# Performance work log

Measured on AMD Instinct MI355X. Metric: run time of the kernel, lower is better.

The kernel has to match this reference:

```python
import jax, jax.numpy as jnp
import numpy as np

L, B, D, H, R, C, WIN = 256, 64, 1024, 512, 8, 6, 10
N = B * L
DH = D + H  # concat(node_features, graph output)


def _window_pairs():
    pi, pk = [], []
    for j in range(L):
        for k in range(max(0, j - WIN), min(L, j + WIN + 1)):
            pi.append(j)
            pk.append(k)
    return np.asarray(pi, np.int32), np.asarray(pk, np.int32)


def setup_inputs() -> dict:
    key = jax.random.key(0)
    ks = jax.random.split(key, 16)
    s = 0.02
    pi, pk = _window_pairs()
    return {
        "features": jax.random.normal(ks[0], (L, B, D), jnp.float32),
        "Wscalar": jax.random.normal(ks[1], (D, L), jnp.float32) * s,   # MaskedEdgeAttention scalar
        "W_rel": jax.random.normal(ks[2], (R, D, H), jnp.float32) * s,  # RGCN per-relation weights
        "W_root": jax.random.normal(ks[3], (D, H), jnp.float32) * s,
        "b_rgcn": jnp.zeros((H,), jnp.float32),
        "W_nbr": jax.random.normal(ks[4], (H, H), jnp.float32) * s,     # GraphConv neighbor weight
        "W_self": jax.random.normal(ks[5], (H, H), jnp.float32) * s,
        "b_gc": jnp.zeros((H,), jnp.float32),
        "W_match": jax.random.normal(ks[6], (DH, DH), jnp.float32) * s,  # MatchingAttention 'general2'
        "b_match": jnp.zeros((DH,), jnp.float32),
        "W_lin": jax.random.normal(ks[7], (DH, H), jnp.float32) * s,
        "b_lin": jnp.zeros((H,), jnp.float32),
        "W_fc": jax.random.normal(ks[8], (H, C), jnp.float32) * s,
        "b_fc": jnp.zeros((C,), jnp.float32),
        "speakers": jax.random.randint(ks[9], (L, B), 0, 2, jnp.int32),
        "pair_i": jnp.asarray(pi),
        "pair_k": jnp.asarray(pk),
    }


def reference(features, Wscalar, W_rel, W_root, b_rgcn, W_nbr, W_self, b_gc,
              W_match, b_match, W_lin, b_lin, W_fc, b_fc,
              speakers, pair_i, pair_k):
    # --- edge attention scores (MaskedEdgeAttention, attn1 style) ---
    scale = jnp.einsum('sbd,dm->sbm', features, Wscalar)      # [L,B,L]
    alpha = jax.nn.softmax(scale, axis=0)
    alpha = jnp.transpose(alpha, (1, 2, 0))                   # [B, anchor, src]
    win = jnp.full((L, L), 1e-10, jnp.float32).at[pair_i, pair_k].set(1.0)
    masked = alpha * win
    scores = masked / jnp.sum(masked, axis=-1, keepdims=True)  # renormalized over window
    edge_norm = scores[:, pair_i, pair_k].reshape(-1)          # [E]

    # --- batch_graphify: flatten nodes conversation-major, build global edges ---
    x = jnp.transpose(features, (1, 0, 2)).reshape(N, D)       # [N, D]
    offs = jnp.arange(B, dtype=jnp.int32)[:, None] * L
    src = (offs + pair_i[None, :]).reshape(-1)
    dst = (offs + pair_k[None, :]).reshape(-1)
    sp = speakers.T                                            # [B, L]
    dir_bit = jnp.where(pair_i < pair_k, 0, 1).astype(jnp.int32)
    rel = (sp[:, pair_i] * 4 + sp[:, pair_k] * 2 + dir_bit[None, :]).reshape(-1)

    # --- RGCNConv: per-relation transform, edge_norm-weighted sum at dst + root ---
    h_all = jnp.einsum('nd,rdh->nrh', x, W_rel)                # [N, R, H]
    msg = h_all[src, rel] * edge_norm[:, None]                 # [E, H]
    agg = jax.ops.segment_sum(msg, dst, num_segments=N)
    h1 = agg + x @ W_root + b_rgcn

    # --- GraphConv: W_nbr @ sum_j x_j + W_self @ x + b ---
    nbr = jax.ops.segment_sum(h1[src], dst, num_segments=N)
    h2 = nbr @ W_nbr + h1 @ W_self + b_gc

    # --- attentive_node_features (MatchingAttention 'general2', full-length mask=1) ---
    em = jnp.concatenate([x, h2], axis=-1).reshape(B, L, DH)
    em = jnp.transpose(em, (1, 0, 2))                          # [L, B, DH] seq-major
    xt = jnp.einsum('tbd,de->tbe', em, W_match) + b_match
    a = jax.nn.softmax(jnp.tanh(jnp.einsum('tbe,sbe->bts', xt, em)), axis=2)
    att = jnp.einsum('bts,sbd->tbd', a, em)                    # [L, B, DH]

    # --- classify_node_features (dropout = eval identity) ---
    hidden = jax.nn.relu(jnp.einsum('tbd,dh->tbh', att, W_lin) + b_lin)
    logp = jax.nn.log_softmax(hidden @ W_fc + b_fc, axis=2)    # [L, B, C]
    return jnp.transpose(logp, (1, 0, 2)).reshape(N, C)
```

## Files before the change

### kernel.cpp

```cpp
#include <hip/hip_runtime.h>
#include <hip/hip_bf16.h>

#define Lc 256
#define Bc 64
#define Dc 1024
#define Hc 512
#define Rc 8
#define Cc 6
#define WINc 10
#define NWc 21
#define Nc (Bc*Lc)
#define DHc (Dc+Hc)
#define CH 8192

typedef __attribute__((ext_vector_type(8))) short short8;
typedef __attribute__((ext_vector_type(4))) float floatx4;

__device__ inline unsigned short f2b(float x) {
    __hip_bfloat16 h = __float2bfloat16(x);
    return *reinterpret_cast<unsigned short*>(&h);
}
__device__ inline float bf2f(unsigned short u) {
    __hip_bfloat16 h;
    *reinterpret_cast<unsigned short*>(&h) = u;
    return __bfloat162float(h);
}

__device__ inline long remap_row(int node) { return (long)(((node & 255) << 6) + (node >> 8)); }

typedef __attribute__((address_space(3))) unsigned int lds_u32;
typedef __attribute__((address_space(1))) unsigned int glb_u32;
__device__ inline void glds16(const unsigned short* g, unsigned short* l) {
    __builtin_amdgcn_global_load_lds((const glb_u32*)g, (lds_u32*)l, 16, 0, 0);
}

#define SB0 __builtin_amdgcn_sched_barrier(0)
#define BAR __builtin_amdgcn_s_barrier()

__device__ __forceinline__ void xcd_remap(int gridX, int& x, int& y)
{
    int nwg = gridDim.x * gridDim.y;
    int bid = blockIdx.y * gridDim.x + blockIdx.x;
    int q = nwg >> 3, r = nwg & 7;
    int xcd = bid & 7, pos = bid >> 3;
    int logical = xcd * q + min(xcd, r) + pos;
    x = logical % gridX;
    y = logical / gridX;
}

__global__ __launch_bounds__(256) void prep_all(
    const float* __restrict__ Wscalar, const float* __restrict__ W_rel,
    const float* __restrict__ W_root, const float* __restrict__ W_nbr,
    const float* __restrict__ W_self, const float* __restrict__ W_match,
    const float* __restrict__ W_lin, unsigned short* __restrict__ WT,
    const int* __restrict__ spk, int* __restrict__ idx, int* __restrict__ cnts,
    const float* __restrict__ feats, unsigned short* __restrict__ em)
{
    int t = blockIdx.x;
    if (t >= 8448 + 16384) {
        int c = t - (8448 + 16384);
        int tid = threadIdx.x;
        int base = c * CH;
        __shared__ int zs[256];
        int zcount = 0;
        for (int i = 0; i < CH / 256; i++) {
            int n = base + tid * (CH / 256) + i;
            if (spk[(n & 255) * 64 + (n >> 8)] == 0) zcount++;
        }
        zs[tid] = zcount; __syncthreads();
        for (int off = 1; off < 256; off <<= 1) {
            int v = (tid >= off) ? zs[tid - off] : 0;
            __syncthreads();
            zs[tid] += v;
            __syncthreads();
        }
        int Z = zs[255];
        int zpos = zs[tid] - zcount;
        int opos = tid * (CH / 256) - zpos;
        for (int i = 0; i < CH / 256; i++) {
            int nl = tid * (CH / 256) + i;
            int n = base + nl;
            if (spk[(n & 255) * 64 + (n >> 8)] == 0) idx[base + (zpos++)] = nl;
            else                                     idx[base + Z + (opos++)] = nl;
        }
        if (tid == 0) cnts[c] = Z;
        return;
    }
    if (t >= 8448) {
        int n = t - 8448;
        int tid = threadIdx.x;
        const float* f = feats + remap_row(n) * Dc;
        float4 v = ((const float4*)f)[tid];
        unsigned short* e = em + (long)n * DHc + tid * 4;
        e[0] = f2b(v.x); e[1] = f2b(v.y); e[2] = f2b(v.z); e[3] = f2b(v.w);
        return;
    }
    const float* in; unsigned short* out; int N, ldo, n0, k0;
    if (t < 256) {
        in = Wscalar; out = WT; N = 256; ldo = 1024;
        n0 = (t & 7) * 32; k0 = (t >> 3) * 32;
    } else if (t < 4352) {
        int u = t - 256; int r = u >> 9; u &= 511;
        in = W_rel + (long)r * 524288; out = WT + 262144 + (long)r * 524288; N = 512; ldo = 1024;
        n0 = (u & 15) * 32; k0 = (u >> 4) * 32;
    } else if (t < 4864) {
        int u = t - 4352;
        in = W_root; out = WT + 262144 + 4096 * 1024; N = 512; ldo = 1024;
        n0 = (u & 15) * 32; k0 = (u >> 4) * 32;
    } else if (t < 5120) {
        int u = t - 4864;
        in = W_nbr; out = WT + 4980736; N = 512; ldo = 1024;
        n0 = (u & 15) * 32; k0 = (u >> 4) * 32;
    } else if (t < 5376) {
        int u = t - 5120;
        in = W_self; out = WT + 4980736 + 512; N = 512; ldo = 1024;
        n0 = (u & 15) * 32; k0 = (u >> 4) * 32;
    } else if (t < 7680) {
        int u = t - 5376;
        in = W_match; out = WT + 5505024; N = 1536; ldo = 1536;
        n0 = (u % 48) * 32; k0 = (u / 48) * 32;
    } else {
        int u = t - 7680;
        in = W_lin; out = WT + 7864320; N = 512; ldo = 1536;
        n0 = (u & 15) * 32; k0 = (u >> 4) * 32;
    }
    __shared__ float tt[32][33];
    int tx = threadIdx.x & 31, ty = threadIdx.x >> 5;
    #pragma unroll
    for (int i = 0; i < 4; i++) tt[ty + i * 8][tx] = in[(long)(k0 + ty + i * 8) * N + n0 + tx];
    __syncthreads();
    #pragma unroll
    for (int i = 0; i < 4; i++) out[(long)(n0 + ty + i * 8) * ldo + k0 + tx] = f2b(tt[tx][ty + i * 8]);
}

template<bool CBF, bool CT, bool BIAS, bool RELU>
__global__ __launch_bounds__(256) void gemm_as(
    const unsigned short* __restrict__ A, const unsigned short* __restrict__ B,
    void* __restrict__ Cv, const float* __restrict__ bias,
    int K, int lda, int ldb, int ldc, long sA, long sB, long sC)
{
    __shared__ __align__(16) unsigned short As[4096];
    __shared__ __align__(16) unsigned short Bs[4096];
    const int tid = threadIdx.x;
    const int z = blockIdx.z;
    const int m0 = blockIdx.y * 128, n0 = blockIdx.x * 128;
    const int lane = tid & 63, wave = tid >> 6;
    const int q = lane >> 4, mr = lane & 15;
    const int wrow = (wave >> 1) * 64, wcol = (wave & 1) * 64;

    const unsigned short* Ag0 = A + z * sA + (long)(m0 + wave * 32 + mr) * lda + q * 8;
    const unsigned short* Ag1 = Ag0 + (long)16 * lda;
    const unsigned short* Bg0 = B + z * sB + (long)(n0 + wave * 32 + mr) * ldb + q * 8;
    const unsigned short* Bg1 = Bg0 + (long)16 * ldb;
    unsigned short* Al0 = As + wave * 1024;
    unsigned short* Bl0 = Bs + wave * 1024;

    floatx4 acc[4][4];
    #pragma unroll
    for (int mt = 0; mt < 4; mt++)
        #pragma unroll
        for (int nt = 0; nt < 4; nt++) acc[mt][nt] = (floatx4){0.f, 0.f, 0.f, 0.f};

    const int ga = (wave >> 1) * 2048;
    const int gb = (wave & 1) * 2048;

    for (int k0 = 0; k0 < K; k0 += 32) {
        glds16(Ag0 + k0, Al0);
        glds16(Ag1 + k0, Al0 + 512);
        glds16(Bg0 + k0, Bl0);
        glds16(Bg1 + k0, Bl0 + 512);
        __syncthreads();
        short8 af[4], bfr[4];
        #pragma unroll
        for (int t = 0; t < 4; t++) {
            af[t]  = *(const short8*)&As[ga + t * 512 + lane * 8];
            bfr[t] = *(const short8*)&Bs[gb + t * 512 + lane * 8];
        }
        #pragma unroll
        for (int mt = 0; mt < 4; mt++)
            #pragma unroll
            for (int nt = 0; nt < 4; nt++)
                acc[mt][nt] = __builtin_amdgcn_mfma_f32_16x16x32_bf16(af[mt], bfr[nt], acc[mt][nt], 0, 0, 0);
        __syncthreads();
    }

    float* Cf = (float*)Cv;
    unsigned short* Cb = (unsigned short*)Cv;
    #pragma unroll
    for (int mt = 0; mt < 4; mt++) {
        #pragma unroll
        for (int nt = 0; nt < 4; nt++) {
            int col = n0 + wcol + nt * 16 + mr;
            float bv = BIAS ? bias[col] : 0.f;
            #pragma unroll
            for (int rg = 0; rg < 4; rg++) {
                int row = m0 + wrow + mt * 16 + q * 4 + rg;
                float v = acc[mt][nt][rg] + bv;
                if (RELU) v = fmaxf(v, 0.f);
                if (CT) {
                    Cb[(long)(row >> 8) * 131072 + (long)col * 256 + (row & 255)] = f2b(v);
                } else {
                    long ci = z * sC + (long)row * ldc + col;
                    if (CBF) Cb[ci] = f2b(v);
                    else     Cf[ci] = v;
                }
            }
        }
    }
}

#define MFMA16(ACCBASE, AFR, BFR) \
    { _Pragma("unroll") \
      for (int mt = 0; mt < 4; mt++) \
        _Pragma("unroll") \
        for (int nt = 0; nt < 4; nt++) \
            acc[ACCBASE + mt][nt] = __builtin_amdgcn_mfma_f32_16x16x32_bf16(AFR[mt], BFR[nt], acc[ACCBASE + mt][nt], 0, 0, 0); }

__device__ __forceinline__ void gemm256_loop(
    unsigned short* lp,
    const unsigned short* Ag0, const unsigned short* Ag1,
    const unsigned short* Bg0, const unsigned short* Bg1,
    int NT, int wofs, const int* offA, const int* offB, floatx4 (&acc)[8][4])
{
    unsigned short* Bl = lp + 32768;
    glds16(Ag0,      lp + wofs);                glds16(Ag1,      lp + wofs + 4096);
    glds16(Ag0 + 32, lp + 8192 + wofs);         glds16(Ag1 + 32, lp + 8192 + wofs + 4096);
    glds16(Bg0,      Bl + wofs);                glds16(Bg1,      Bl + wofs + 4096);
    glds16(Bg0 + 32, Bl + 8192 + wofs);         glds16(Bg1 + 32, Bl + 8192 + wofs + 4096);
    glds16(Bg0 + 64, Bl + 16384 + wofs);        glds16(Bg1 + 64, Bl + 16384 + wofs + 4096);
    glds16(Bg0 + 96, Bl + 16384 + 8192 + wofs); glds16(Bg1 + 96, Bl + 16384 + 8192 + wofs + 4096);
    glds16(Ag0 + 64, lp + 16384 + wofs);        glds16(Ag1 + 64, lp + 16384 + wofs + 4096);
    asm volatile("s_waitcnt vmcnt(6)" ::: "memory");

    short8 aF[4], bQ[4], b2Q[4];
    for (int t = 0; t < NT; t++) {
        const int buf = t & 1;
        const int ab  = buf * 16384;
        const int abx = (buf ^ 1) * 16384;

        SB0; BAR; SB0;
        #pragma unroll
        for (int i = 0; i < 4; i++) aF[i] = *(const short8*)(lp + ab + offA[i]);
        #pragma unroll
        for (int i = 0; i < 4; i++) bQ[i] = *(const short8*)(Bl + ab + offB[i]);
        if (t + 1 < NT) {
            const int kc = (t + 1) * 64 + 32;
            glds16(Ag0 + kc, lp + abx + 8192 + wofs);
            glds16(Ag1 + kc, lp + abx + 8192 + wofs + 4096);
        }
        asm volatile("s_waitcnt lgkmcnt(0)" ::: "memory"); SB0;
        __builtin_amdgcn_s_setprio(1);
        MFMA16(0, aF, bQ)
        __builtin_amdgcn_s_setprio(0);

        SB0; BAR; SB0;
        #pragma unroll
        for (int i = 0; i < 4; i++) aF[i]  = *(const short8*)(lp + ab + offA[4 + i]);
        #pragma unroll
        for (int i = 0; i < 4; i++) b2Q[i] = *(const short8*)(Bl + ab + 8192 + offB[i]);
        if (t + 2 < NT) {
            const int kc = (t + 2) * 64;
            glds16(Bg0 + kc, Bl + ab + wofs);
            glds16(Bg1 + kc, Bl + ab + wofs + 4096);
        }
        asm volatile("s_waitcnt lgkmcnt(0)" ::: "memory"); SB0;
        __builtin_amdgcn_s_setprio(1);
        MFMA16(4, aF, bQ)
        __builtin_amdgcn_s_setprio(0);

        SB0; BAR; SB0;
        #pragma unroll
        for (int i = 0; i < 4; i++) aF[i] = *(const short8*)(lp + ab + 8192 + offA[i]);
        if (t + 2 < NT) {
            const int kc = (t + 2) * 64 + 32;
            glds16(Bg0 + kc, Bl + ab + 8192 + wofs);
            glds16(Bg1 + kc, Bl + ab + 8192 + wofs + 4096);
        }
        asm volatile("s_waitcnt lgkmcnt(0)" ::: "memory"); SB0;
        __builtin_amdgcn_s_setprio(1);
        MFMA16(0, aF, b2Q)
        __builtin_amdgcn_s_setprio(0);

        SB0; BAR; SB0;
        #pragma unroll
        for (int i = 0; i < 4; i++) aF[i] = *(const short8*)(lp + ab + 8192 + offA[4 + i]);
        if (t + 2 < NT) {
            const int kc = (t + 2) * 64;
            glds16(Ag0 + kc, lp + ab + wofs);
            glds16(Ag1 + kc, lp + ab + wofs + 4096);
        }
        if (t < NT - 2)       { asm volatile("s_waitcnt vmcnt(6)" ::: "memory"); }
        else if (t == NT - 2) { asm volatile("s_waitcnt vmcnt(0)" ::: "memory"); }
        asm volatile("s_waitcnt lgkmcnt(0)" ::: "memory"); SB0;
        __builtin_amdgcn_s_setprio(1);
        MFMA16(4, aF, b2Q)
        __builtin_amdgcn_s_setprio(0);
    }
}

__device__ __forceinline__ void frag_offsets(int wm, int wn, int q, int mr, int* offA, int* offB)
{
    #pragma unroll
    for (int mt = 0; mt < 8; mt++) {
        int row = wm * 128 + mt * 16 + mr;
        offA[mt] = row * 32 + ((q ^ ((row >> 1) & 3)) * 8);
    }
    #pragma unroll
    for (int nt = 0; nt < 4; nt++) {
        int row = wn * 64 + nt * 16 + mr;
        offB[nt] = row * 32 + ((q ^ ((row >> 1) & 3)) * 8);
    }
}

template<bool CBF, bool CT, bool BIAS, bool RELU>
__global__ __launch_bounds__(512, 2) void gemm256(
    const unsigned short* __restrict__ A, const unsigned short* __restrict__ B,
    void* __restrict__ Cv, const float* __restrict__ bias,
    int K, int lda, int ldb, int ldc)
{
    __shared__ __align__(16) unsigned short LDS[65536];
    unsigned short* lp = &LDS[0];
    const int tid  = threadIdx.x;
    const int lane = tid & 63, wave = tid >> 6;
    const int wm = wave >> 2, wn = wave & 3;
    int bx, by;
    xcd_remap(gridDim.x, bx, by);
    const int m0 = by * 256, n0 = bx * 256;
    const int NT = K >> 6;
    const int q = lane >> 4, mr = lane & 15;

    const int r0 = wave * 16 + (lane >> 2);
    const int r1 = r0 + 128;
    const int c0 = ((lane & 3) ^ ((r0 >> 1) & 3)) * 8;
    const int c1 = ((lane & 3) ^ ((r1 >> 1) & 3)) * 8;
    const unsigned short* Ag0 = A + (long)(m0 + r0) * lda + c0;
    const unsigned short* Ag1 = A + (long)(m0 + r1) * lda + c1;
    const unsigned short* Bg0 = B + (long)(n0 + r0) * ldb + c0;
    const unsigned short* Bg1 = B + (long)(n0 + r1) * ldb + c1;
    const int wofs = wave * 512;

    int offA[8], offB[4];
    frag_offsets(wm, wn, q, mr, offA, offB);

    floatx4 acc[8][4];
    #pragma unroll
    for (int mt = 0; mt < 8; mt++)
        #pragma unroll
        for (int nt = 0; nt < 4; nt++) acc[mt][nt] = (floatx4){0.f, 0.f, 0.f, 0.f};

    gemm256_loop(lp, Ag0, Ag1, Bg0, Bg1, NT, wofs, offA, offB, acc);

    float* Cf = (float*)Cv;
    unsigned short* Cb = (unsigned short*)Cv;
    #pragma unroll
    for (int mt = 0; mt < 8; mt++) {
        #pragma unroll
        for (int nt = 0; nt < 4; nt++) {
            int col = n0 + wn * 64 + nt * 16 + mr;
            float bv = BIAS ? bias[col] : 0.f;
            #pragma unroll
            for (int rg = 0; rg < 4; rg++) {
                int row = m0 + wm * 128 + mt * 16 + q * 4 + rg;
                float v = acc[mt][nt][rg] + bv;
                if (RELU) v = fmaxf(v, 0.f);
                if (CT) {
                    Cb[(long)(row >> 8) * 131072 + (long)col * 256 + (row & 255)] = f2b(v);
                } else {
                    long ci = (long)row * ldc + col;
                    if (CBF) Cb[ci] = f2b(v);
                    else     Cf[ci] = v;
                }
            }
        }
    }
}

__global__ __launch_bounds__(512, 2) void rgcn256(
    const unsigned short* __restrict__ A, const unsigned short* __restrict__ B,
    unsigned short* __restrict__ C, const int* __restrict__ idx,
    const int* __restrict__ cntp)
{
    const int cnt0 = *cntp;
    const int t0 = (cnt0 + 255) >> 8;
    const int M1 = CH - cnt0;
    const int t1 = (M1 + 255) >> 8;
    int x, ty;
    xcd_remap(gridDim.x, x, ty);
    int sblk, m0, M, off;
    if (ty < t0)           { sblk = 0; m0 = ty << 8;        M = cnt0; off = 0; }
    else if (ty < t0 + t1) { sblk = 1; m0 = (ty - t0) << 8; M = M1;   off = cnt0; }
    else return;

    const int brow = ((x < 8) ? sblk * 2048 : 2048) + x * 256;

    __shared__ __align__(16) unsigned short LDS[65536];
    unsigned short* lp = &LDS[0];
    const int tid  = threadIdx.x;
    const int lane = tid & 63, wave = tid >> 6;
    const int wm = wave >> 2, wn = wave & 3;
    const int q = lane >> 4, mr = lane & 15;

    const int r0 = wave * 16 + (lane >> 2);
    const int r1 = r0 + 128;
    const int c0 = ((lane & 3) ^ ((r0 >> 1) & 3)) * 8;
    const int c1 = ((lane & 3) ^ ((r1 >> 1) & 3)) * 8;
    const int gr0 = idx[off + min(m0 + r0, M - 1)];
    const int gr1 = idx[off + min(m0 + r1, M - 1)];
    const unsigned short* Ag0 = A + (long)gr0 * DHc + c0;
    const unsigned short* Ag1 = A + (long)gr1 * DHc + c1;
    const unsigned short* Bg0 = B + (long)(brow + r0) * 1024 + c0;
    const unsigned short* Bg1 = B + (long)(brow + r1) * 1024 + c1;
    const int wofs = wave * 512;

    int offA[8], offB[4];
    frag_offsets(wm, wn, q, mr, offA, offB);

    floatx4 acc[8][4];
    #pragma unroll
    for (int mt = 0; mt < 8; mt++)
        #pragma unroll
        for (int nt = 0; nt < 4; nt++) acc[mt][nt] = (floatx4){0.f, 0.f, 0.f, 0.f};

    gemm256_loop(lp, Ag0, Ag1, Bg0, Bg1, 16 , wofs, offA, offB, acc);

    #pragma unroll
    for (int mt = 0; mt < 8; mt++) {
        int rowb = m0 + wm * 128 + mt * 16 + q * 4;
        int cr[4];
        #pragma unroll
        for (int rg = 0; rg < 4; rg++) cr[rg] = idx[off + min(rowb + rg, M - 1)];
        #pragma unroll
        for (int nt = 0; nt < 4; nt++) {
            int col = x * 256 + wn * 64 + nt * 16 + mr;
            #pragma unroll
            for (int rg = 0; rg < 4; rg++)
                C[(long)cr[rg] * 2560 + col] = f2b(acc[mt][nt][rg]);
        }
    }
}

__global__ __launch_bounds__(512, 2) void gemm256_mw(
    const unsigned short* __restrict__ A, const unsigned short* __restrict__ B,
    unsigned short* __restrict__ xt, unsigned short* __restrict__ emWT,
    const float* __restrict__ b_match, const float* __restrict__ b_lin)
{
    __shared__ __align__(16) unsigned short LDS[65536];
    unsigned short* lp = &LDS[0];
    const int tid  = threadIdx.x;
    const int lane = tid & 63, wave = tid >> 6;
    const int wm = wave >> 2, wn = wave & 3;
    int bx, by;
    xcd_remap(gridDim.x, bx, by);
    const int m0 = by * 256, n0 = bx * 256;
    const int q = lane >> 4, mr = lane & 15;

    const int r0 = wave * 16 + (lane >> 2);
    const int r1 = r0 + 128;
    const int c0 = ((lane & 3) ^ ((r0 >> 1) & 3)) * 8;
    const int c1 = ((lane & 3) ^ ((r1 >> 1) & 3)) * 8;
    const unsigned short* Ag0 = A + (long)(m0 + r0) * DHc + c0;
    const unsigned short* Ag1 = A + (long)(m0 + r1) * DHc + c1;
    const unsigned short* Bg0 = B + (long)(n0 + r0) * 1536 + c0;
    const unsigned short* Bg1 = B + (long)(n0 + r1) * 1536 + c1;
    const int wofs = wave * 512;

    int offA[8], offB[4];
    frag_offsets(wm, wn, q, mr, offA, offB);

    floatx4 acc[8][4];
    #pragma unroll
    for (int mt = 0; mt < 8; mt++)
        #pragma unroll
        for (int nt = 0; nt < 4; nt++) acc[mt][nt] = (floatx4){0.f, 0.f, 0.f, 0.f};

    gemm256_loop(lp, Ag0, Ag1, Bg0, Bg1, 24 , wofs, offA, offB, acc);

    if (n0 < 1536) {
        #pragma unroll
        for (int mt = 0; mt < 8; mt++) {
            #pragma unroll
            for (int nt = 0; nt < 4; nt++) {
                int col = n0 + wn * 64 + nt * 16 + mr;
                float bv = b_match[col];
                #pragma unroll
                for (int rg = 0; rg < 4; rg++) {
                    int row = m0 + wm * 128 + mt * 16 + q * 4 + rg;
                    xt[(long)row * DHc + col] = f2b(acc[mt][nt][rg] + bv);
                }
            }
        }
    } else {
        #pragma unroll
        for (int mt = 0; mt < 8; mt++) {
            #pragma unroll
            for (int nt = 0; nt < 4; nt++) {
                int col = (n0 - 1536) + wn * 64 + nt * 16 + mr;
                float bv = b_lin[col];
                #pragma unroll
                for (int rg = 0; rg < 4; rg++) {
                    int row = m0 + wm * 128 + mt * 16 + q * 4 + rg;
                    emWT[(long)(row >> 8) * 131072 + (long)col * 256 + (row & 255)] =
                        f2b(acc[mt][nt][rg] + bv);
                }
            }
        }
    }
}

__global__ __launch_bounds__(256) void edge_norm_kernel(const float* __restrict__ scale,
                                                        float* __restrict__ enorm)
{
    int g = blockIdx.x * 256 + threadIdx.x;
    int b = g >> 8, j = g & 255;
    int klo = max(0, j - WINc), khi = min(Lc - 1, j + WINc);
    float vals[NWc];
    float m = -1e30f;
    for (int k = klo; k <= khi; k++) {
        float v = scale[(long)((b << 8) + k) * Lc + j];
        vals[k - klo] = v;
        m = fmaxf(m, v);
    }
    float s = 0.f;
    for (int k = klo; k <= khi; k++) {
        float e = expf(vals[k - klo] - m);
        vals[k - klo] = e;
        s += e;
    }
    float inv = 1.f / s;
    for (int k = klo; k <= khi; k++)
        enorm[(long)g * NWc + (k - j + WINc)] = vals[k - klo] * inv;
}

__global__ __launch_bounds__(256) void rgcn_gather4(const unsigned short* __restrict__ hall4,
        const float* __restrict__ enorm, const int* __restrict__ spk,
        const float* __restrict__ b_rgcn, float* __restrict__ h1, int chunk_base)
{
    int nloc = blockIdx.x;
    int n = chunk_base + nloc;
    int b = n >> 8, k = n & 255;
    int tid = threadIdx.x;
    int spkk = spk[k * 64 + b];
    int jlo = max(0, k - WINc), jhi = min(Lc - 1, k + WINc);
    unsigned int ru = *(const unsigned int*)(hall4 + (long)nloc * 2560 + 2048 + 2 * tid);
    float a0 = bf2f((unsigned short)(ru & 0xffff)) + b_rgcn[2 * tid];
    float a1 = bf2f((unsigned short)(ru >> 16)) + b_rgcn[2 * tid + 1];
    int cb = spkk * 2;
    for (int j = jlo; j <= jhi; j++) {
        int c = cb + ((j < k) ? 0 : 1);
        float w = enorm[((long)((b << 8) + j)) * NWc + (k - j + WINc)];
        unsigned int u = *(const unsigned int*)(hall4 + ((long)(nloc - k + j)) * 2560 + c * 512 + 2 * tid);
        a0 += w * bf2f((unsigned short)(u & 0xffff));
        a1 += w * bf2f((unsigned short)(u >> 16));
    }
    *(float2*)&h1[(long)n * Hc + 2 * tid] = make_float2(a0, a1);
}

__global__ __launch_bounds__(256) void build_anh1(const float* __restrict__ h1,
                                                  unsigned short* __restrict__ anh1)
{
    int n = blockIdx.x;
    int b = n >> 8, k = n & 255;
    int tid = threadIdx.x;
    int jlo = max(0, k - WINc), jhi = min(Lc - 1, k + WINc);
    float a0 = 0.f, a1 = 0.f;
    for (int j = jlo; j <= jhi; j++) {
        const float* src = h1 + ((long)((b << 8) + j)) * Hc;
        a0 += src[tid];
        a1 += src[tid + 256];
    }
    unsigned short* dst = anh1 + (long)n * 1024;
    const float* self = h1 + (long)n * Hc;
    dst[tid]       = f2b(a0);
    dst[tid + 256] = f2b(a1);
    dst[tid + 512] = f2b(self[tid]);
    dst[tid + 768] = f2b(self[tid + 256]);
}

__global__ __launch_bounds__(256) void tanh_softmax_rows(const float* __restrict__ S,
                                                         unsigned short* __restrict__ a)
{
    int row = blockIdx.x;
    int tid = threadIdx.x;
    __shared__ float red[256];
    float v = tanhf(S[(long)row * Lc + tid]);
    red[tid] = v; __syncthreads();
    for (int s = 128; s > 0; s >>= 1) { if (tid < s) red[tid] = fmaxf(red[tid], red[tid + s]); __syncthreads(); }
    float m = red[0]; __syncthreads();
    float e = expf(v - m);
    red[tid] = e; __syncthreads();
    for (int s = 128; s > 0; s >>= 1) { if (tid < s) red[tid] += red[tid + s]; __syncthreads(); }
    float sum = red[0];
    a[(long)row * Lc + tid] = f2b(e / sum);
}

__global__ __launch_bounds__(256) void out_kernel(const unsigned short* __restrict__ hidden,
        const float* __restrict__ Wfc, const float* __restrict__ bfc, float* __restrict__ out)
{
    int tid = threadIdx.x;
    int lane = tid & 63;
    int row = blockIdx.x * 4 + (tid >> 6);
    float acc[Cc] = {};
    const unsigned short* h = hidden + (long)row * Hc;
    for (int k = lane; k < Hc; k += 64) {
        float hv = bf2f(h[k]);
        #pragma unroll
        for (int c = 0; c < Cc; c++) acc[c] += hv * Wfc[k * Cc + c];
    }
    #pragma unroll
    for (int c = 0; c < Cc; c++)
        for (int off = 32; off > 0; off >>= 1) acc[c] += __shfl_down(acc[c], off, 64);
    if (lane == 0) {
        float m = -1e30f;
        #pragma unroll
        for (int c = 0; c < Cc; c++) { acc[c] += bfc[c]; m = fmaxf(m, acc[c]); }
        float s = 0.f;
        #pragma unroll
        for (int c = 0; c < Cc; c++) s += expf(acc[c] - m);
        float lse = logf(s);
        #pragma unroll
        for (int c = 0; c < Cc; c++) out[(long)row * Cc + c] = acc[c] - m - lse;
    }
}

extern "C" void kernel_launch(void* const* d_in, const int* in_sizes, int n_in,
                              void* d_out, int out_size, void* d_ws, size_t ws_size,
                              hipStream_t stream)
{
    const float* feats   = (const float*)d_in[0];
    const float* Wscalar = (const float*)d_in[1];
    const float* W_rel   = (const float*)d_in[2];
    const float* W_root  = (const float*)d_in[3];
    const float* b_rgcn  = (const float*)d_in[4];
    const float* W_nbr   = (const float*)d_in[5];
    const float* W_self  = (const float*)d_in[6];
    const float* b_gc    = (const float*)d_in[7];
    const float* W_match = (const float*)d_in[8];
    const float* b_match = (const float*)d_in[9];
    const float* W_lin   = (const float*)d_in[10];
    const float* b_lin   = (const float*)d_in[11];
    const float* W_fc    = (const float*)d_in[12];
    const float* b_fc    = (const float*)d_in[13];
    const int*   spk     = (const int*)d_in[14];

    char* wsb = (char*)d_ws;
    unsigned short* em    = (unsigned short*)wsb;
    char* RB = wsb + 50331648;
    float*          scale = (float*)RB;
    unsigned short* hall4 = (unsigned short*)RB;
    unsigned short* anh1  = (unsigned short*)RB;
    unsigned short* xt    = (unsigned short*)RB;
    unsigned short* hidden= (unsigned short*)(RB + 16777216);
    char* HB = wsb + 100663296;
    float*          h1    = (float*)HB;
    float*          S     = (float*)HB;
    unsigned short* emWT  = (unsigned short*)(wsb + 117440512);
    int* idx              = (int*)(HB + 16777216);
    int* cnts             = (int*)(HB + 16777216 + 65536);
    unsigned short* WT    = (unsigned short*)(wsb + 134217728);
    unsigned short* WscalarT = WT;
    unsigned short* WrelT    = WT + 262144;
    unsigned short* WgcT     = WT + 4980736;
    unsigned short* WmatchT  = WT + 5505024;
    unsigned short* ac    = (unsigned short*)(wsb + 134217728);
    float*          enorm = (float*)(wsb + 151519232);

    prep_all<<<dim3(8448 + 16384 + 2), 256, 0, stream>>>(
        Wscalar, W_rel, W_root, W_nbr, W_self, W_match, W_lin, WT,
        spk, idx, cnts, feats, em);

    gemm_as<false, false, false, false><<<dim3(2, 128, 1), 256, 0, stream>>>(
        em, WscalarT, scale, nullptr, 1024, DHc, 1024, 256, 0, 0, 0);

    edge_norm_kernel<<<dim3(64), 256, 0, stream>>>(scale, enorm);

    for (int c = 0; c < 2; c++) {
        const unsigned short* emc = em + (long)c * CH * DHc;
        rgcn256<<<dim3(10, 33, 1), 512, 0, stream>>>(
            emc, WrelT, hall4, idx + c * CH, cnts + c);
        rgcn_gather4<<<dim3(CH), 256, 0, stream>>>(hall4, enorm, spk, b_rgcn, h1, c * CH);
    }

    build_anh1<<<dim3(Nc), 256, 0, stream>>>(h1, anh1);
    gemm256<true, false, true, false><<<dim3(2, 64, 1), 512, 0, stream>>>(
        anh1, WgcT, em + 1024, b_gc, 1024, 1024, 1024, DHc);

    gemm256_mw<<<dim3(8, 64, 1), 512, 0, stream>>>(
        em, WmatchT, xt, emWT, b_match, b_lin);

    gemm_as<false, false, false, false><<<dim3(2, 2, 64), 256, 0, stream>>>(
        xt, em, S, nullptr, DHc, DHc, DHc, 256, 393216, 393216, 65536);

    tanh_softmax_rows<<<dim3(Nc), 256, 0, stream>>>(S, ac);

    gemm_as<true, false, false, true><<<dim3(4, 2, 64), 256, 0, stream>>>(
        ac, emWT, hidden, nullptr, 256, 256, 256, 512, 65536, 131072, 131072);

    out_kernel<<<dim3(Nc / 4), 256, 0, stream>>>(hidden, W_fc, b_fc, (float*)d_out);
}
```

Baseline: 694.2 us.

## Stage RGCN gather and neighbor-sum inputs in shared memory per conversation strip

Replaces the per-node gather and neighbor-sum kernels with block-per-(column strip, conversation) kernels. Each block loads a whole conversation's column slice into LDS using direct global-to-LDS loads, then computes the banded window sums from shared memory. Each global row is then read once per block instead of about 21 times from L2. The cost is much larger LDS use per block, which lowers occupancy, and fewer, heavier blocks.

```diff
diff --git a/kernel.cpp b/kernel.cpp
--- a/kernel.cpp
+++ b/kernel.cpp
@@ -531,49 +531,87 @@
         enorm[(long)g * NWc + (k - j + WINc)] = vals[k - klo] * inv;
 }
 
-__global__ __launch_bounds__(256) void rgcn_gather4(const unsigned short* __restrict__ hall4,
-        const float* __restrict__ enorm, const int* __restrict__ spk,
-        const float* __restrict__ b_rgcn, float* __restrict__ h1, int chunk_base)
-{
-    int nloc = blockIdx.x;
-    int n = chunk_base + nloc;
-    int b = n >> 8, k = n & 255;
-    int tid = threadIdx.x;
-    int spkk = spk[k * 64 + b];
-    int jlo = max(0, k - WINc), jhi = min(Lc - 1, k + WINc);
-    unsigned int ru = *(const unsigned int*)(hall4 + (long)nloc * 2560 + 2048 + 2 * tid);
-    float a0 = bf2f((unsigned short)(ru & 0xffff)) + b_rgcn[2 * tid];
-    float a1 = bf2f((unsigned short)(ru >> 16)) + b_rgcn[2 * tid + 1];
-    int cb = spkk * 2;
-    for (int j = jlo; j <= jhi; j++) {
-        int c = cb + ((j < k) ? 0 : 1);
-        float w = enorm[((long)((b << 8) + j)) * NWc + (k - j + WINc)];
-        unsigned int u = *(const unsigned int*)(hall4 + ((long)(nloc - k + j)) * 2560 + c * 512 + 2 * tid);
-        a0 += w * bf2f((unsigned short)(u & 0xffff));
-        a1 += w * bf2f((unsigned short)(u >> 16));
-    }
-    *(float2*)&h1[(long)n * Hc + 2 * tid] = make_float2(a0, a1);
-}
-
-__global__ __launch_bounds__(256) void build_anh1(const float* __restrict__ h1,
-                                                  unsigned short* __restrict__ anh1)
-{
-    int n = blockIdx.x;
-    int b = n >> 8, k = n & 255;
-    int tid = threadIdx.x;
-    int jlo = max(0, k - WINc), jhi = min(Lc - 1, k + WINc);
-    float a0 = 0.f, a1 = 0.f;
-    for (int j = jlo; j <= jhi; j++) {
-        const float* src = h1 + ((long)((b << 8) + j)) * Hc;
-        a0 += src[tid];
-        a1 += src[tid + 256];
-    }
-    unsigned short* dst = anh1 + (long)n * 1024;
-    const float* self = h1 + (long)n * Hc;
-    dst[tid]       = f2b(a0);
-    dst[tid + 256] = f2b(a1);
-    dst[tid + 512] = f2b(self[tid]);
-    dst[tid + 768] = f2b(self[tid + 256]);
+__global__ __launch_bounds__(512) void rgcn_gather256(
+    const unsigned short* __restrict__ hall4, const float* __restrict__ enorm,
+    const int* __restrict__ spk, const float* __restrict__ b_rgcn,
+    float* __restrict__ h1, int chunk_base)
+{
+    __shared__ __align__(16) unsigned short hs[40960];
+    __shared__ float ws[5376];
+    __shared__ int spkS[256];
+    const int strip = blockIdx.x;
+    const int conv  = blockIdx.y;
+    const int b     = (chunk_base >> 8) + conv;
+    const int tid = threadIdx.x, lane = tid & 63, wave = tid >> 6;
+
+    #pragma unroll
+    for (int cId = 0; cId < 10; cId++) {
+        int segBase = cId * 128 + wave * 16;
+        int seg = segBase + (lane >> 2);
+        int c = seg >> 8, r = seg & 255;
+        long src = ((long)conv * 256 + r) * 2560 + (c < 4 ? c * 512 : 2048)
+                 + strip * 32 + (lane & 3) * 8;
+        glds16(hall4 + src, hs + segBase * 32);
+    }
+    const float* en = enorm + (((long)b << 8)) * NWc;
+    for (int i = tid; i < 5376; i += 512) ws[i] = en[i];
+    if (tid < 256) spkS[tid] = spk[tid * Bc + b];
+    __syncthreads();
+
+    const int p = tid & 15;
+    const int kbase = (tid >> 4) * 8;
+    const int colg = strip * 32 + p * 2;
+    const float bb0 = b_rgcn[colg], bb1 = b_rgcn[colg + 1];
+    for (int kk = 0; kk < 8; kk++) {
+        int k = kbase + kk;
+        int jlo = max(0, k - WINc), jhi = min(Lc - 1, k + WINc);
+        unsigned int ru = *(const unsigned int*)(hs + (1024 + k) * 32 + p * 2);
+        float a0 = bf2f((unsigned short)(ru & 0xffff)) + bb0;
+        float a1 = bf2f((unsigned short)(ru >> 16)) + bb1;
+        int cb = spkS[k] * 2;
+        for (int j = jlo; j <= jhi; j++) {
+            int c = cb + ((j < k) ? 0 : 1);
+            float w = ws[j * NWc + (k - j + WINc)];
+            unsigned int u = *(const unsigned int*)(hs + (c * 256 + j) * 32 + p * 2);
+            a0 += w * bf2f((unsigned short)(u & 0xffff));
+            a1 += w * bf2f((unsigned short)(u >> 16));
+        }
+        long n = (long)chunk_base + conv * 256 + k;
+        *(float2*)&h1[n * Hc + colg] = make_float2(a0, a1);
+    }
+}
+
+__global__ __launch_bounds__(512) void build_anh256(const float* __restrict__ h1,
+                                                    unsigned short* __restrict__ anh1)
+{
+    __shared__ __align__(16) float hsf[32768];
+    const int strip = blockIdx.x;
+    const int conv  = blockIdx.y;
+    const int tid = threadIdx.x, lane = tid & 63, wave = tid >> 6;
+
+    #pragma unroll
+    for (int cId = 0; cId < 16; cId++) {
+        int segBase = cId * 128 + wave * 16;
+        int seg = segBase + (lane >> 2);
+        int r = seg >> 3, sc = seg & 7;
+        const float* src = h1 + ((long)conv * 256 + r) * Hc + strip * 128 + sc * 16 + (lane & 3) * 4;
+        glds16((const unsigned short*)src, (unsigned short*)(hsf + segBase * 16));
+    }
+    __syncthreads();
+
+    const int col = tid & 127;
+    const int kbase = (tid >> 7) * 64;
+    const int colg = strip * 128 + col;
+    for (int kk = 0; kk < 64; kk++) {
+        int k = kbase + kk;
+        int jlo = max(0, k - WINc), jhi = min(Lc - 1, k + WINc);
+        float a = 0.f;
+        for (int j = jlo; j <= jhi; j++) a += hsf[j * 128 + col];
+        float self = hsf[k * 128 + col];
+        unsigned short* dst = anh1 + ((long)conv * 256 + k) * 1024;
+        dst[colg] = f2b(a);
+        dst[512 + colg] = f2b(self);
+    }
 }
 
 __global__ __launch_bounds__(256) void tanh_softmax_rows(const float* __restrict__ S,
@@ -677,10 +715,11 @@
         const unsigned short* emc = em + (long)c * CH * DHc;
         rgcn256<<<dim3(10, 33, 1), 512, 0, stream>>>(
             emc, WrelT, hall4, idx + c * CH, cnts + c);
-        rgcn_gather4<<<dim3(CH), 256, 0, stream>>>(hall4, enorm, spk, b_rgcn, h1, c * CH);
-    }
-
-    build_anh1<<<dim3(Nc), 256, 0, stream>>>(h1, anh1);
+        rgcn_gather256<<<dim3(16, 32, 1), 512, 0, stream>>>(
+            hall4, enorm, spk, b_rgcn, h1, c * CH);
+    }
+
+    build_anh256<<<dim3(4, 64, 1), 512, 0, stream>>>(h1, anh1);
     gemm256<true, false, true, false><<<dim3(2, 64, 1), 512, 0, stream>>>(
         anh1, WgcT, em + 1024, b_gc, 1024, 1024, 1024, DHc);
 
```

After: 706.8 us. Within noise of the previous version (+1.8%).
